# Performance work log

Measured on AMD Instinct MI355X. Metric: run time of the kernel, lower is better.

Reference implementation:

```python
import jax, jax.numpy as jnp
import numpy as np
from jax import lax

B, T, D, U = 64, 512, 512, 1024


def setup_inputs() -> dict:
    key = jax.random.key(0)
    k1, k2, k3 = jax.random.split(key, 3)
    x = jax.random.normal(k1, (B, T, D), dtype=jnp.float32)
    # Keras LSTM parameters: kernel [D,4U], recurrent kernel [U,4U], bias [4U]
    W = jax.random.normal(k2, (D, 4 * U), dtype=jnp.float32) * 0.02
    R = jax.random.normal(k3, (U, 4 * U), dtype=jnp.float32) * 0.02
    b = jnp.zeros((4 * U,), dtype=jnp.float32)
    return {"x": x, "W": W, "R": R, "b": b}


def _lstm_last(x, W, R, b):
    # Precompute input projections for all timesteps: [B,T,4U]
    xW = jnp.einsum('btd,dk->btk', x, W) + b
    h0 = jnp.zeros((x.shape[0], U), dtype=x.dtype)
    c0 = jnp.zeros((x.shape[0], U), dtype=x.dtype)

    def step(carry, xw_t):
        h, c = carry
        z = xw_t + h @ R                      # [B,4U]
        i, f, g, o = jnp.split(z, 4, axis=-1)  # Keras gate order i,f,c,o
        i = jax.nn.sigmoid(i)
        f = jax.nn.sigmoid(f)
        g = jnp.tanh(g)
        o = jax.nn.sigmoid(o)
        c_new = f * c + i * g
        h_new = o * jnp.tanh(c_new)
        return (h_new, c_new), None

    (h_last, _), _ = lax.scan(step, (h0, c0), jnp.swapaxes(xW, 0, 1))
    return h_last  # return_sequences=False -> last hidden state [B,U]


def reference(x, W, R, b):
    return _lstm_last(x, W, R, b)
```

## Files before the change

kernel.cpp:

```cpp
#include <hip/hip_runtime.h>
#include <hip/hip_bf16.h>
#include <stdint.h>

#define BB 64
#define TT 512
#define DD 512
#define UU 1024
#define G4 4096
#define RETRY_CAP 16384

typedef __bf16 bf16x8 __attribute__((ext_vector_type(8)));
typedef float f32x4 __attribute__((ext_vector_type(4)));
typedef unsigned short u16x8 __attribute__((ext_vector_type(8)));
typedef int i32x4 __attribute__((ext_vector_type(4)));
typedef unsigned int u32;

__device__ __forceinline__ unsigned short f2bf(float f) {
  unsigned u = __builtin_bit_cast(unsigned, f);
  return (unsigned short)((u + 0x7FFFu + ((u >> 16) & 1u)) >> 16);
}

__global__ void cvt_x_kernel(const float* __restrict__ x, unsigned short* __restrict__ xb, int n8) {
  int i = blockIdx.x * blockDim.x + threadIdx.x;
  if (i >= n8) return;
  const float4* p = reinterpret_cast<const float4*>(x) + (size_t)i * 2;
  float4 a = p[0], b = p[1];
  u16x8 o;
  o[0] = f2bf(a.x); o[1] = f2bf(a.y); o[2] = f2bf(a.z); o[3] = f2bf(a.w);
  o[4] = f2bf(b.x); o[5] = f2bf(b.y); o[6] = f2bf(b.z); o[7] = f2bf(b.w);
  reinterpret_cast<u16x8*>(xb)[i] = o;
}

__global__ void zero_kernel(u32* __restrict__ p, int nwords) {
  for (int i = blockIdx.x * blockDim.x + threadIdx.x; i < nwords; i += gridDim.x * blockDim.x) {
    u32 z = 0u;
    const u32* q = p + i;
    asm volatile("global_store_dword %0, %1, off sc0 sc1" :: "v"(q), "v"(z) : "memory");
  }
}

__launch_bounds__(512, 1)
__global__ void lstm_persist(const float* __restrict__ W, const float* __restrict__ R,
                             const float* __restrict__ bias,
                             const unsigned short* __restrict__ xb,
                             u32* __restrict__ hbuf,
                             float* __restrict__ out) {
  __shared__ float zone[2 * 8 * 4 * 4 * 64];

  const int bid = blockIdx.x;
  const int bgrp = bid >> 6;
  const int m = bid & 63;
  const int tid = threadIdx.x;
  const int w = tid >> 6;
  const int lane = tid & 63, l15 = lane & 15, lk = lane >> 4;
  const int rb = w & 1, rsel = w >> 1;
  const int u0 = m * 16;

  bf16x8 Wf[2][4];
  bf16x8 Rf[4][4];
  #pragma unroll
  for (int g = 0; g < 4; ++g) {
    const int gcol = g * 1024 + u0 + l15;
    #pragma unroll
    for (int s = 0; s < 2; ++s) {
      const int k0 = w * 64 + s * 32 + lk * 8;
      u16x8 tmp;
      #pragma unroll
      for (int j = 0; j < 8; ++j) tmp[j] = f2bf(W[(size_t)(k0 + j) * G4 + gcol]);
      Wf[s][g] = __builtin_bit_cast(bf16x8, tmp);
    }
    #pragma unroll
    for (int s = 0; s < 4; ++s) {
      const int k0 = w * 128 + s * 32 + lk * 8;
      u16x8 tmp;
      #pragma unroll
      for (int j = 0; j < 8; ++j) tmp[j] = f2bf(R[(size_t)(k0 + j) * G4 + gcol]);
      Rf[s][g] = __builtin_bit_cast(bf16x8, tmp);
    }
  }
  float bv[4];
  #pragma unroll
  for (int g = 0; g < 4; ++g) bv[g] = bias[g * 1024 + u0 + l15];

  float cst = 0.f;

  const unsigned short* xr0 = xb + (size_t)(bgrp * 32 + 0 + l15) * (TT * DD) + w * 64 + lk * 8;
  const unsigned short* xr1 = xb + (size_t)(bgrp * 32 + 16 + l15) * (TT * DD) + w * 64 + lk * 8;
  u32* hbg = hbuf + (size_t)bgrp * 2 * 32 * UU;
  const u32* hrA0 = hbg + (size_t)(0 + l15) * UU + w * 128 + lk * 8;
  const u32* hrA1 = hbg + (size_t)(16 + l15) * UU + w * 128 + lk * 8;
  const u32* hrB0 = hrA0 + 32 * UU;
  const u32* hrB1 = hrA1 + 32 * UU;
  u32* hsA = hbg + (size_t)(rb * 16 + lk * 4 + rsel) * UU + u0 + l15;
  u32* hsB = hsA + 32 * UU;

  asm volatile("s_waitcnt vmcnt(0)" ::: "memory");
  __builtin_amdgcn_sched_barrier(0);

  i32x4 H0[2][2], H1[2][2];

#define HISSUE(Harr, S)                                                          \
  {                                                                              \
    const u32* p0 = b0 + (S) * 32;                                               \
    const u32* p1 = b1 + (S) * 32;                                               \
    asm volatile(                                                                \
        "global_load_dwordx4 %0, %4, off sc0 sc1\n\t"                            \
        "global_load_dwordx4 %1, %4, off offset:16 sc0 sc1\n\t"                  \
        "global_load_dwordx4 %2, %5, off sc0 sc1\n\t"                            \
        "global_load_dwordx4 %3, %5, off offset:16 sc0 sc1"                      \
        : "=&v"(Harr[0][0]), "=&v"(Harr[0][1]), "=&v"(Harr[1][0]), "=&v"(Harr[1][1]) \
        : "v"(p0), "v"(p1)                                                       \
        : "memory");                                                             \
  }

#define VBAD(Harr, badv)                                                         \
  {                                                                              \
    badv = 0;                                                                    \
    _Pragma("unroll") for (int rl = 0; rl < 2; ++rl)                             \
        _Pragma("unroll") for (int q = 0; q < 2; ++q)                            \
            _Pragma("unroll") for (int d = 0; d < 4; ++d)                        \
                badv |= (Harr[rl][q][d] ^ t) & 0xFFFF;                           \
  }

#define VSTEP(Harr, S, VC)                                                       \
  {                                                                              \
    asm volatile("s_waitcnt vmcnt(" #VC ")" ::: "memory");                       \
    __builtin_amdgcn_sched_barrier(0);                                           \
    int bad;                                                                     \
    VBAD(Harr, bad);                                                             \
    int rtry = 0;                                                                \
    while (__any(bad != 0) && ++rtry < RETRY_CAP) {                              \
      HISSUE(Harr, S);                                                           \
      asm volatile("s_waitcnt vmcnt(0)" ::: "memory");                           \
      __builtin_amdgcn_sched_barrier(0);                                         \
      VBAD(Harr, bad);                                                           \
    }                                                                            \
    _Pragma("unroll") for (int rl = 0; rl < 2; ++rl) {                           \
      i32x4 fr;                                                                  \
      fr[0] = __builtin_amdgcn_perm(Harr[rl][0][1], Harr[rl][0][0], 0x07060302); \
      fr[1] = __builtin_amdgcn_perm(Harr[rl][0][3], Harr[rl][0][2], 0x07060302); \
      fr[2] = __builtin_amdgcn_perm(Harr[rl][1][1], Harr[rl][1][0], 0x07060302); \
      fr[3] = __builtin_amdgcn_perm(Harr[rl][1][3], Harr[rl][1][2], 0x07060302); \
      _Pragma("unroll") for (int g = 0; g < 4; ++g)                              \
          acc[rl][g] = __builtin_amdgcn_mfma_f32_16x16x32_bf16(                  \
              __builtin_bit_cast(bf16x8, fr), Rf[S][g], acc[rl][g], 0, 0, 0);    \
    }                                                                            \
  }

  #pragma unroll 1
  for (int t = 0; t < TT; ++t) {
    const int zb = t & 1;
    f32x4 acc[2][4];
    #pragma unroll
    for (int rl = 0; rl < 2; ++rl)
      #pragma unroll
      for (int g = 0; g < 4; ++g) acc[rl][g] = f32x4{0.f, 0.f, 0.f, 0.f};

    i32x4 Ax[2][2];
    asm volatile(
        "global_load_dwordx4 %0, %4, off\n\t"
        "global_load_dwordx4 %1, %4, off offset:64\n\t"
        "global_load_dwordx4 %2, %5, off\n\t"
        "global_load_dwordx4 %3, %5, off offset:64"
        : "=&v"(Ax[0][0]), "=&v"(Ax[0][1]), "=&v"(Ax[1][0]), "=&v"(Ax[1][1])
        : "v"(xr0), "v"(xr1));
    xr0 += DD; xr1 += DD;

    const u32* b0 = zb ? hrB0 : hrA0;
    const u32* b1 = zb ? hrB1 : hrA1;

    if (t > 0) {
      HISSUE(H0, 0);
      HISSUE(H1, 1);
      asm volatile("s_waitcnt vmcnt(8)" ::: "memory");
      __builtin_amdgcn_sched_barrier(0);
    } else {
      asm volatile("s_waitcnt vmcnt(0)" ::: "memory");
      __builtin_amdgcn_sched_barrier(0);
    }

    #pragma unroll
    for (int s = 0; s < 2; ++s)
      #pragma unroll
      for (int rl = 0; rl < 2; ++rl)
        #pragma unroll
        for (int g = 0; g < 4; ++g)
          acc[rl][g] = __builtin_amdgcn_mfma_f32_16x16x32_bf16(
              __builtin_bit_cast(bf16x8, Ax[rl][s]), Wf[s][g], acc[rl][g], 0, 0, 0);

    if (t > 0) {
      VSTEP(H0, 0, 4); HISSUE(H0, 2);
      VSTEP(H1, 1, 4); HISSUE(H1, 3);
      VSTEP(H0, 2, 4);
      VSTEP(H1, 3, 0);
    }

    __syncthreads();
    #pragma unroll
    for (int rl = 0; rl < 2; ++rl)
      #pragma unroll
      for (int g = 0; g < 4; ++g)
        #pragma unroll
        for (int c = 0; c < 4; ++c)
          zone[((((rl * 8 + w) * 4 + g) * 4 + c) << 6) + lane] = acc[rl][g][c];
    __syncthreads();

    float z[4];
    #pragma unroll
    for (int g = 0; g < 4; ++g) {
      float s = bv[g];
      #pragma unroll
      for (int src = 0; src < 8; ++src)
        s += zone[((((rb * 8 + src) * 4 + g) * 4 + rsel) << 6) + lane];
      z[g] = s;
    }
    const float ig = 1.f / (1.f + __expf(-z[0]));
    const float fg = 1.f / (1.f + __expf(-z[1]));
    const float gg = 1.f - 2.f / (1.f + __expf(2.f * z[2]));
    const float og = 1.f / (1.f + __expf(-z[3]));
    const float c = fg * cst + ig * gg;
    cst = c;
    const float h = og * (1.f - 2.f / (1.f + __expf(2.f * c)));

    if (t < TT - 1) {
      const u32 hw = ((u32)f2bf(h) << 16) | (u32)(t + 1);
      u32* hs = zb ? hsA : hsB;
      asm volatile("global_store_dword %0, %1, off sc0 sc1" :: "v"(hs), "v"(hw) : "memory");
    } else {
      out[(size_t)(bgrp * 32 + rb * 16 + lk * 4 + rsel) * UU + u0 + l15] = h;
    }
  }
#undef HISSUE
#undef VBAD
#undef VSTEP
}

extern "C" void kernel_launch(void* const* d_in, const int* in_sizes, int n_in,
                              void* d_out, int out_size, void* d_ws, size_t ws_size,
                              hipStream_t stream) {
  const float* x = (const float*)d_in[0];
  const float* W = (const float*)d_in[1];
  const float* R = (const float*)d_in[2];
  const float* b = (const float*)d_in[3];
  float* out = (float*)d_out;

  char* ws = (char*)d_ws;
  unsigned short* xb = (unsigned short*)ws;
  const size_t XB_BYTES = (size_t)BB * TT * DD * 2;
  u32* hbuf = (u32*)(ws + XB_BYTES);
  const int HB_WORDS = 2 * 2 * 32 * UU;

  hipLaunchKernelGGL(cvt_x_kernel, dim3((BB * TT * DD / 8 + 255) / 256), dim3(256), 0, stream,
                     x, xb, BB * TT * DD / 8);
  hipLaunchKernelGGL(zero_kernel, dim3(128), dim3(256), 0, stream, hbuf, HB_WORDS);
  hipLaunchKernelGGL(lstm_persist, dim3(128), dim3(512), 0, stream,
                     W, R, b, xb, hbuf, out);
}
```

Baseline: 3.937 ms.

## Halve persistent grid and pipeline four batch groups per timestep

The persistent LSTM kernel now runs on 64 blocks of 4 waves instead of 128 blocks of 8 waves. Each block owns a 16-unit slice for all 64 batch rows and processes them as four sequential 16-row groups per timestep, so polling for one group's hidden state can overlap with other blocks still producing the next group. Each wave holds a larger K-slice of W and R in registers, and the poll retry loop adds a short sleep with a lower retry cap. The trade-off is roughly three times more MFMA work per SIMD and four block barriers per timestep, against hoped-for lower cross-block synchronization latency.

```diff
diff --git a/kernel.cpp b/kernel.cpp
--- a/kernel.cpp
+++ b/kernel.cpp
@@ -7,20 +7,21 @@
 #define DD 512
 #define UU 1024
 #define G4 4096
-#define RETRY_CAP 16384
+#define RETRY_CAP 8192
 
 typedef __bf16 bf16x8 __attribute__((ext_vector_type(8)));
 typedef float f32x4 __attribute__((ext_vector_type(4)));
-typedef unsigned short u16x8 __attribute__((ext_vector_type(8)));
 typedef int i32x4 __attribute__((ext_vector_type(4)));
 typedef unsigned int u32;
-
-__device__ __forceinline__ unsigned short f2bf(float f) {
+typedef unsigned short u16;
+typedef u16 u16x8 __attribute__((ext_vector_type(8)));
+
+__device__ __forceinline__ u16 f2bf(float f) {
   unsigned u = __builtin_bit_cast(unsigned, f);
-  return (unsigned short)((u + 0x7FFFu + ((u >> 16) & 1u)) >> 16);
-}
-
-__global__ void cvt_x_kernel(const float* __restrict__ x, unsigned short* __restrict__ xb, int n8) {
+  return (u16)((u + 0x7FFFu + ((u >> 16) & 1u)) >> 16);
+}
+
+__global__ void cvt_x_kernel(const float* __restrict__ x, u16* __restrict__ xb, int n8) {
   int i = blockIdx.x * blockDim.x + threadIdx.x;
   if (i >= n8) return;
   const float4* p = reinterpret_cast<const float4*>(x) + (size_t)i * 2;
@@ -39,39 +40,36 @@
   }
 }
 
-__launch_bounds__(512, 1)
+__launch_bounds__(256, 1) __attribute__((amdgpu_waves_per_eu(1, 1)))
 __global__ void lstm_persist(const float* __restrict__ W, const float* __restrict__ R,
-                             const float* __restrict__ bias,
-                             const unsigned short* __restrict__ xb,
+                             const float* __restrict__ bias, const u16* __restrict__ xb,
                              u32* __restrict__ hbuf,
                              float* __restrict__ out) {
-  __shared__ float zone[2 * 8 * 4 * 4 * 64];
+  __shared__ float zone[4 * 4 * 64 * 4];
 
   const int bid = blockIdx.x;
-  const int bgrp = bid >> 6;
-  const int m = bid & 63;
   const int tid = threadIdx.x;
-  const int w = tid >> 6;
-  const int lane = tid & 63, l15 = lane & 15, lk = lane >> 4;
-  const int rb = w & 1, rsel = w >> 1;
-  const int u0 = m * 16;
-
-  bf16x8 Wf[2][4];
-  bf16x8 Rf[4][4];
+  const int w = tid >> 6, lane = tid & 63, l15 = lane & 15, lk = lane >> 4;
+  const int u0 = bid * 16;
+  const int r = tid >> 4;
+  const int uu = tid & 15;
+
+  bf16x8 Wf[4][4];
+  bf16x8 Rf[8][4];
   #pragma unroll
   for (int g = 0; g < 4; ++g) {
     const int gcol = g * 1024 + u0 + l15;
     #pragma unroll
-    for (int s = 0; s < 2; ++s) {
-      const int k0 = w * 64 + s * 32 + lk * 8;
+    for (int s = 0; s < 4; ++s) {
+      const int k0 = w * 128 + s * 32 + lk * 8;
       u16x8 tmp;
       #pragma unroll
       for (int j = 0; j < 8; ++j) tmp[j] = f2bf(W[(size_t)(k0 + j) * G4 + gcol]);
       Wf[s][g] = __builtin_bit_cast(bf16x8, tmp);
     }
     #pragma unroll
-    for (int s = 0; s < 4; ++s) {
-      const int k0 = w * 128 + s * 32 + lk * 8;
+    for (int s = 0; s < 8; ++s) {
+      const int k0 = w * 256 + s * 32 + lk * 8;
       u16x8 tmp;
       #pragma unroll
       for (int j = 0; j < 8; ++j) tmp[j] = f2bf(R[(size_t)(k0 + j) * G4 + gcol]);
@@ -80,159 +78,152 @@
   }
   float bv[4];
   #pragma unroll
-  for (int g = 0; g < 4; ++g) bv[g] = bias[g * 1024 + u0 + l15];
-
-  float cst = 0.f;
-
-  const unsigned short* xr0 = xb + (size_t)(bgrp * 32 + 0 + l15) * (TT * DD) + w * 64 + lk * 8;
-  const unsigned short* xr1 = xb + (size_t)(bgrp * 32 + 16 + l15) * (TT * DD) + w * 64 + lk * 8;
-  u32* hbg = hbuf + (size_t)bgrp * 2 * 32 * UU;
-  const u32* hrA0 = hbg + (size_t)(0 + l15) * UU + w * 128 + lk * 8;
-  const u32* hrA1 = hbg + (size_t)(16 + l15) * UU + w * 128 + lk * 8;
-  const u32* hrB0 = hrA0 + 32 * UU;
-  const u32* hrB1 = hrA1 + 32 * UU;
-  u32* hsA = hbg + (size_t)(rb * 16 + lk * 4 + rsel) * UU + u0 + l15;
-  u32* hsB = hsA + 32 * UU;
+  for (int g = 0; g < 4; ++g) bv[g] = bias[g * 1024 + u0 + uu];
+  float cst[4] = {0.f, 0.f, 0.f, 0.f};
+
+  const u16* xq[4];
+  const u32* hr[4];
+  u32* hs[4];
+  #pragma unroll
+  for (int g = 0; g < 4; ++g) {
+    xq[g] = xb + (size_t)(g * 16 + l15) * (TT * DD) + w * 128 + lk * 8;
+    hr[g] = hbuf + (size_t)(g * 32 + l15) * 1024 + w * 256 + lk * 8;
+    hs[g] = hbuf + (size_t)(g * 32 + r) * 1024 + u0 + uu;
+  }
 
   asm volatile("s_waitcnt vmcnt(0)" ::: "memory");
   __builtin_amdgcn_sched_barrier(0);
 
-  i32x4 H0[2][2], H1[2][2];
-
-#define HISSUE(Harr, S)                                                          \
-  {                                                                              \
-    const u32* p0 = b0 + (S) * 32;                                               \
-    const u32* p1 = b1 + (S) * 32;                                               \
-    asm volatile(                                                                \
-        "global_load_dwordx4 %0, %4, off sc0 sc1\n\t"                            \
-        "global_load_dwordx4 %1, %4, off offset:16 sc0 sc1\n\t"                  \
-        "global_load_dwordx4 %2, %5, off sc0 sc1\n\t"                            \
-        "global_load_dwordx4 %3, %5, off offset:16 sc0 sc1"                      \
-        : "=&v"(Harr[0][0]), "=&v"(Harr[0][1]), "=&v"(Harr[1][0]), "=&v"(Harr[1][1]) \
-        : "v"(p0), "v"(p1)                                                       \
-        : "memory");                                                             \
-  }
-
-#define VBAD(Harr, badv)                                                         \
-  {                                                                              \
-    badv = 0;                                                                    \
-    _Pragma("unroll") for (int rl = 0; rl < 2; ++rl)                             \
-        _Pragma("unroll") for (int q = 0; q < 2; ++q)                            \
-            _Pragma("unroll") for (int d = 0; d < 4; ++d)                        \
-                badv |= (Harr[rl][q][d] ^ t) & 0xFFFF;                           \
-  }
-
-#define VSTEP(Harr, S, VC)                                                       \
-  {                                                                              \
-    asm volatile("s_waitcnt vmcnt(" #VC ")" ::: "memory");                       \
-    __builtin_amdgcn_sched_barrier(0);                                           \
-    int bad;                                                                     \
-    VBAD(Harr, bad);                                                             \
-    int rtry = 0;                                                                \
-    while (__any(bad != 0) && ++rtry < RETRY_CAP) {                              \
-      HISSUE(Harr, S);                                                           \
-      asm volatile("s_waitcnt vmcnt(0)" ::: "memory");                           \
-      __builtin_amdgcn_sched_barrier(0);                                         \
-      VBAD(Harr, bad);                                                           \
-    }                                                                            \
-    _Pragma("unroll") for (int rl = 0; rl < 2; ++rl) {                           \
-      i32x4 fr;                                                                  \
-      fr[0] = __builtin_amdgcn_perm(Harr[rl][0][1], Harr[rl][0][0], 0x07060302); \
-      fr[1] = __builtin_amdgcn_perm(Harr[rl][0][3], Harr[rl][0][2], 0x07060302); \
-      fr[2] = __builtin_amdgcn_perm(Harr[rl][1][1], Harr[rl][1][0], 0x07060302); \
-      fr[3] = __builtin_amdgcn_perm(Harr[rl][1][3], Harr[rl][1][2], 0x07060302); \
-      _Pragma("unroll") for (int g = 0; g < 4; ++g)                              \
-          acc[rl][g] = __builtin_amdgcn_mfma_f32_16x16x32_bf16(                  \
-              __builtin_bit_cast(bf16x8, fr), Rf[S][g], acc[rl][g], 0, 0, 0);    \
-    }                                                                            \
-  }
+  i32x4 H[8][2], Ax[4];
+  f32x4 acc[4];
+
+#define HISSUE(HQ)                                                             \
+  asm volatile(                                                                \
+      "global_load_dwordx4 %0, %16, off sc0 sc1\n\t"                           \
+      "global_load_dwordx4 %1, %16, off offset:16 sc0 sc1\n\t"                 \
+      "global_load_dwordx4 %2, %16, off offset:128 sc0 sc1\n\t"                \
+      "global_load_dwordx4 %3, %16, off offset:144 sc0 sc1\n\t"                \
+      "global_load_dwordx4 %4, %16, off offset:256 sc0 sc1\n\t"                \
+      "global_load_dwordx4 %5, %16, off offset:272 sc0 sc1\n\t"                \
+      "global_load_dwordx4 %6, %16, off offset:384 sc0 sc1\n\t"                \
+      "global_load_dwordx4 %7, %16, off offset:400 sc0 sc1\n\t"                \
+      "global_load_dwordx4 %8, %16, off offset:512 sc0 sc1\n\t"                \
+      "global_load_dwordx4 %9, %16, off offset:528 sc0 sc1\n\t"                \
+      "global_load_dwordx4 %10, %16, off offset:640 sc0 sc1\n\t"               \
+      "global_load_dwordx4 %11, %16, off offset:656 sc0 sc1\n\t"               \
+      "global_load_dwordx4 %12, %16, off offset:768 sc0 sc1\n\t"               \
+      "global_load_dwordx4 %13, %16, off offset:784 sc0 sc1\n\t"               \
+      "global_load_dwordx4 %14, %16, off offset:896 sc0 sc1\n\t"               \
+      "global_load_dwordx4 %15, %16, off offset:912 sc0 sc1"                   \
+      : "=&v"(H[0][0]), "=&v"(H[0][1]), "=&v"(H[1][0]), "=&v"(H[1][1]),        \
+        "=&v"(H[2][0]), "=&v"(H[2][1]), "=&v"(H[3][0]), "=&v"(H[3][1]),        \
+        "=&v"(H[4][0]), "=&v"(H[4][1]), "=&v"(H[5][0]), "=&v"(H[5][1]),        \
+        "=&v"(H[6][0]), "=&v"(H[6][1]), "=&v"(H[7][0]), "=&v"(H[7][1])         \
+      : "v"(HQ) : "memory")
+
+#define VBAD(badv)                                                             \
+  badv = 0;                                                                    \
+  _Pragma("unroll") for (int s_ = 0; s_ < 8; ++s_)                             \
+    _Pragma("unroll") for (int q_ = 0; q_ < 2; ++q_)                           \
+      _Pragma("unroll") for (int d_ = 0; d_ < 4; ++d_)                         \
+        badv |= (H[s_][q_][d_] ^ t) & 0xFFFF
 
   #pragma unroll 1
   for (int t = 0; t < TT; ++t) {
-    const int zb = t & 1;
-    f32x4 acc[2][4];
-    #pragma unroll
-    for (int rl = 0; rl < 2; ++rl)
-      #pragma unroll
-      for (int g = 0; g < 4; ++g) acc[rl][g] = f32x4{0.f, 0.f, 0.f, 0.f};
-
-    i32x4 Ax[2][2];
-    asm volatile(
-        "global_load_dwordx4 %0, %4, off\n\t"
-        "global_load_dwordx4 %1, %4, off offset:64\n\t"
-        "global_load_dwordx4 %2, %5, off\n\t"
-        "global_load_dwordx4 %3, %5, off offset:64"
-        : "=&v"(Ax[0][0]), "=&v"(Ax[0][1]), "=&v"(Ax[1][0]), "=&v"(Ax[1][1])
-        : "v"(xr0), "v"(xr1));
-    xr0 += DD; xr1 += DD;
-
-    const u32* b0 = zb ? hrB0 : hrA0;
-    const u32* b1 = zb ? hrB1 : hrA1;
-
-    if (t > 0) {
-      HISSUE(H0, 0);
-      HISSUE(H1, 1);
-      asm volatile("s_waitcnt vmcnt(8)" ::: "memory");
-      __builtin_amdgcn_sched_barrier(0);
-    } else {
-      asm volatile("s_waitcnt vmcnt(0)" ::: "memory");
-      __builtin_amdgcn_sched_barrier(0);
-    }
-
-    #pragma unroll
-    for (int s = 0; s < 2; ++s)
-      #pragma unroll
-      for (int rl = 0; rl < 2; ++rl)
-        #pragma unroll
-        for (int g = 0; g < 4; ++g)
-          acc[rl][g] = __builtin_amdgcn_mfma_f32_16x16x32_bf16(
-              __builtin_bit_cast(bf16x8, Ax[rl][s]), Wf[s][g], acc[rl][g], 0, 0, 0);
-
-    if (t > 0) {
-      VSTEP(H0, 0, 4); HISSUE(H0, 2);
-      VSTEP(H1, 1, 4); HISSUE(H1, 3);
-      VSTEP(H0, 2, 4);
-      VSTEP(H1, 3, 0);
-    }
-
-    __syncthreads();
-    #pragma unroll
-    for (int rl = 0; rl < 2; ++rl)
-      #pragma unroll
-      for (int g = 0; g < 4; ++g)
-        #pragma unroll
-        for (int c = 0; c < 4; ++c)
-          zone[((((rl * 8 + w) * 4 + g) * 4 + c) << 6) + lane] = acc[rl][g][c];
-    __syncthreads();
-
-    float z[4];
+    const int pr = (t & 1) * 16384;
+    const int pw = ((t + 1) & 1) * 16384;
+
     #pragma unroll
     for (int g = 0; g < 4; ++g) {
-      float s = bv[g];
-      #pragma unroll
-      for (int src = 0; src < 8; ++src)
-        s += zone[((((rb * 8 + src) * 4 + g) * 4 + rsel) << 6) + lane];
-      z[g] = s;
-    }
-    const float ig = 1.f / (1.f + __expf(-z[0]));
-    const float fg = 1.f / (1.f + __expf(-z[1]));
-    const float gg = 1.f - 2.f / (1.f + __expf(2.f * z[2]));
-    const float og = 1.f / (1.f + __expf(-z[3]));
-    const float c = fg * cst + ig * gg;
-    cst = c;
-    const float h = og * (1.f - 2.f / (1.f + __expf(2.f * c)));
-
-    if (t < TT - 1) {
-      const u32 hw = ((u32)f2bf(h) << 16) | (u32)(t + 1);
-      u32* hs = zb ? hsA : hsB;
-      asm volatile("global_store_dword %0, %1, off sc0 sc1" :: "v"(hs), "v"(hw) : "memory");
-    } else {
-      out[(size_t)(bgrp * 32 + rb * 16 + lk * 4 + rsel) * UU + u0 + l15] = h;
+      asm volatile(
+          "global_load_dwordx4 %0, %4, off\n\t"
+          "global_load_dwordx4 %1, %4, off offset:64\n\t"
+          "global_load_dwordx4 %2, %4, off offset:128\n\t"
+          "global_load_dwordx4 %3, %4, off offset:192"
+          : "=&v"(Ax[0]), "=&v"(Ax[1]), "=&v"(Ax[2]), "=&v"(Ax[3])
+          : "v"(xq[g]));
+      xq[g] += DD;
+
+      const u32* hq = hr[g] + pr;
+      if (t > 0) {
+        HISSUE(hq);
+        asm volatile("s_waitcnt vmcnt(16)" ::: "memory");
+      } else {
+        asm volatile("s_waitcnt vmcnt(0)" ::: "memory");
+      }
+      __builtin_amdgcn_sched_barrier(0);
+
+      #pragma unroll
+      for (int f = 0; f < 4; ++f) acc[f] = f32x4{0.f, 0.f, 0.f, 0.f};
+
+      #pragma unroll
+      for (int s = 0; s < 4; ++s)
+        #pragma unroll
+        for (int f = 0; f < 4; ++f)
+          acc[f] = __builtin_amdgcn_mfma_f32_16x16x32_bf16(
+              __builtin_bit_cast(bf16x8, Ax[s]), Wf[s][f], acc[f], 0, 0, 0);
+
+      if (t > 0) {
+        asm volatile("s_waitcnt vmcnt(0)" ::: "memory");
+        __builtin_amdgcn_sched_barrier(0);
+        int bad;
+        VBAD(bad);
+        int rtry = 0;
+        while (__any(bad != 0) && ++rtry < RETRY_CAP) {
+          __builtin_amdgcn_s_sleep(2);
+          HISSUE(hq);
+          asm volatile("s_waitcnt vmcnt(0)" ::: "memory");
+          __builtin_amdgcn_sched_barrier(0);
+          VBAD(bad);
+        }
+        #pragma unroll
+        for (int s = 0; s < 8; ++s) {
+          i32x4 fr;
+          fr[0] = __builtin_amdgcn_perm(H[s][0][1], H[s][0][0], 0x07060302);
+          fr[1] = __builtin_amdgcn_perm(H[s][0][3], H[s][0][2], 0x07060302);
+          fr[2] = __builtin_amdgcn_perm(H[s][1][1], H[s][1][0], 0x07060302);
+          fr[3] = __builtin_amdgcn_perm(H[s][1][3], H[s][1][2], 0x07060302);
+          #pragma unroll
+          for (int f = 0; f < 4; ++f)
+            acc[f] = __builtin_amdgcn_mfma_f32_16x16x32_bf16(
+                __builtin_bit_cast(bf16x8, fr), Rf[s][f], acc[f], 0, 0, 0);
+        }
+      }
+
+      __syncthreads();
+      #pragma unroll
+      for (int f = 0; f < 4; ++f)
+        *(f32x4*)&zone[((w * 4 + f) * 64 + lane) * 4] = acc[f];
+      __syncthreads();
+
+      float z[4];
+      #pragma unroll
+      for (int gg = 0; gg < 4; ++gg) {
+        float s = bv[gg];
+        #pragma unroll
+        for (int ww = 0; ww < 4; ++ww)
+          s += zone[((ww * 4 + gg) * 64 + (r >> 2) * 16 + uu) * 4 + (r & 3)];
+        z[gg] = s;
+      }
+      const float ig = 1.f / (1.f + __expf(-z[0]));
+      const float fg = 1.f / (1.f + __expf(-z[1]));
+      const float gt = 1.f - 2.f / (1.f + __expf(2.f * z[2]));
+      const float og = 1.f / (1.f + __expf(-z[3]));
+      const float c = fg * cst[g] + ig * gt;
+      cst[g] = c;
+      const float h = og * (1.f - 2.f / (1.f + __expf(2.f * c)));
+
+      if (t < TT - 1) {
+        const u32 hwd = ((u32)f2bf(h) << 16) | (u32)(t + 1);
+        u32* hp = hs[g] + pw;
+        asm volatile("global_store_dword %0, %1, off sc0 sc1" :: "v"(hp), "v"(hwd) : "memory");
+      } else {
+        out[(size_t)(g * 16 + r) * UU + u0 + uu] = h;
+      }
     }
   }
 #undef HISSUE
 #undef VBAD
-#undef VSTEP
 }
 
 extern "C" void kernel_launch(void* const* d_in, const int* in_sizes, int n_in,
@@ -245,14 +236,14 @@
   float* out = (float*)d_out;
 
   char* ws = (char*)d_ws;
-  unsigned short* xb = (unsigned short*)ws;
+  u16* xb = (u16*)ws;
   const size_t XB_BYTES = (size_t)BB * TT * DD * 2;
   u32* hbuf = (u32*)(ws + XB_BYTES);
-  const int HB_WORDS = 2 * 2 * 32 * UU;
+  const int HB_WORDS = 4 * 2 * 16 * 1024;
 
   hipLaunchKernelGGL(cvt_x_kernel, dim3((BB * TT * DD / 8 + 255) / 256), dim3(256), 0, stream,
                      x, xb, BB * TT * DD / 8);
-  hipLaunchKernelGGL(zero_kernel, dim3(128), dim3(256), 0, stream, hbuf, HB_WORDS);
-  hipLaunchKernelGGL(lstm_persist, dim3(128), dim3(512), 0, stream,
+  hipLaunchKernelGGL(zero_kernel, dim3(64), dim3(256), 0, stream, hbuf, HB_WORDS);
+  hipLaunchKernelGGL(lstm_persist, dim3(64), dim3(256), 0, stream,
                      W, R, b, xb, hbuf, out);
 }
```

Result: slower. 8.588 ms (+118.1%).
